# Optimization experiments

Measured on AMD Instinct MI355X. Metric: run time of the kernel, lower is better.

The kernel has to match this reference:

```python
import jax, jax.numpy as jnp
import numpy as np

N, D_IN, D_H, D_OUT, R, E, NB = 50000, 128, 128, 64, 4, 400000, 2

def _xavier(k, shape, fan_in, fan_out):
    # torch xavier_uniform with relu gain sqrt(2)
    lim = np.sqrt(2.0) * np.sqrt(6.0 / (fan_in + fan_out))
    return jax.random.uniform(k, shape, jnp.float32, -lim, lim)

def setup_inputs() -> dict:
    key = jax.random.key(0)
    ks = jax.random.split(key, 9)
    x = jax.random.normal(ks[0], (N, D_IN), dtype=jnp.float32)
    src = jax.random.randint(ks[1], (R, E), 0, N, dtype=jnp.int32)
    dst = jax.random.randint(ks[2], (R, E), 0, N, dtype=jnp.int32)
    inp = {"x": x, "src": src, "dst": dst}
    dims = [(D_IN, D_H), (D_H, D_H), (D_H, D_OUT)]
    for i, (di, do) in enumerate(dims):
        inp[f"basis{i}"] = _xavier(ks[3 + 2 * i], (NB, di, do), di, do)
        inp[f"coeff{i}"] = _xavier(ks[4 + 2 * i], (R, NB), NB, R)
    return inp

def _rel_layer(h, src, dst, basis, coeff):
    """One RelGraphConvLayer: per-relation basis weight + GraphConv(norm='both'),
    summed over relations (HeteroGraphConv aggregate='sum')."""
    n = h.shape[0]
    W = jnp.einsum('rb,bio->rio', coeff, basis)  # [R, d_in, d_out] basis-decomposed weights
    out = jnp.zeros((n, W.shape[-1]), dtype=h.dtype)
    for r in range(src.shape[0]):  # fixed small set of relations
        s, d = src[r], dst[r]
        ones = jnp.ones(s.shape[0], dtype=h.dtype)
        deg_out = jnp.maximum(jax.ops.segment_sum(ones, s, num_segments=n), 1.0)
        deg_in = jnp.maximum(jax.ops.segment_sum(ones, d, num_segments=n), 1.0)
        norm_src = deg_out ** -0.5
        norm_dst = deg_in ** -0.5
        # weight applied before aggregation (d_in >= d_out path of dgl GraphConv; math identical)
        hr = (h * norm_src[:, None]) @ W[r]            # [N, d_out]
        agg = jax.ops.segment_sum(hr[s], d, num_segments=n)  # SpMM via gather + scatter-add
        out = out + agg * norm_dst[:, None]
    return out

def reference(x, src, dst, basis0, coeff0, basis1, coeff1, basis2, coeff2):
    h = jax.nn.relu(_rel_layer(x, src, dst, basis0, coeff0))
    h = jax.nn.relu(_rel_layer(h, src, dst, basis1, coeff1))
    return _rel_layer(h, src, dst, basis2, coeff2)  # final layer: no activation
```

## Files before the change

kernel.cpp:

```cpp
#include <hip/hip_runtime.h>
#include <hip/hip_bf16.h>
#include <cstdint>
#include <cstddef>

#define NN 50000
#define RR 4
#define EE 400000
#define TE (RR*EE)
#define HR 12500
#define RN (RR*NN)
#define NSEG (NN*RR)
#define SCB2 782
#define NBK 512
#define BKSZ 98
#define CHA 4000
#define MAXSPAN 4608

using frag_ab = __attribute__((ext_vector_type(8))) short;
using frag_cd = __attribute__((ext_vector_type(4))) float;

static __device__ __forceinline__ unsigned short f2bf(float f) {
    union { float f; unsigned u; } v; v.f = f;
    unsigned r = (v.u + 0x7FFF + ((v.u >> 16) & 1)) >> 16;
    return (unsigned short)r;
}
static __device__ __forceinline__ unsigned pack2(float lo, float hi) {
    return (unsigned)f2bf(lo) | ((unsigned)f2bf(hi) << 16);
}
static __device__ __forceinline__ float blo(unsigned u) { return __uint_as_float(u << 16); }
static __device__ __forceinline__ float bhi(unsigned u) { return __uint_as_float(u & 0xFFFF0000u); }

__global__ __launch_bounds__(1024) void k_hist(const int* __restrict__ src,
                                               const int* __restrict__ dst,
                                               int* __restrict__ cnt_srcQ,
                                               int* __restrict__ cnt_dstQ) {
    __shared__ unsigned bins[HR / 2];
    int combo = blockIdx.x >> 4;
    int range = (blockIdx.x >> 2) & 3;
    int qc    = blockIdx.x & 3;
    int r = combo >> 1;
    int side = combo & 1;
    const int* arr = (side == 0 ? src : dst) + (size_t)r * EE + (size_t)qc * (EE / 4);
    int lo = range * HR;
    for (int i = threadIdx.x; i < HR / 2; i += 1024) bins[i] = 0;
    __syncthreads();
    const int4* a4 = (const int4*)arr;
    for (int i = threadIdx.x; i < EE / 16; i += 1024) {
        int4 v = a4[i];
        int t;
        t = v.x - lo; if ((unsigned)t < (unsigned)HR) atomicAdd(&bins[t >> 1], 1u << ((t & 1) * 16));
        t = v.y - lo; if ((unsigned)t < (unsigned)HR) atomicAdd(&bins[t >> 1], 1u << ((t & 1) * 16));
        t = v.z - lo; if ((unsigned)t < (unsigned)HR) atomicAdd(&bins[t >> 1], 1u << ((t & 1) * 16));
        t = v.w - lo; if ((unsigned)t < (unsigned)HR) atomicAdd(&bins[t >> 1], 1u << ((t & 1) * 16));
    }
    __syncthreads();
    int* outp = (side == 0 ? cnt_srcQ : cnt_dstQ) + (size_t)qc * RN + (size_t)r * NN + lo;
    for (int i = threadIdx.x; i < HR / 2; i += 1024) {
        unsigned b = bins[i];
        outp[2 * i]     = (int)(b & 0xFFFFu);
        outp[2 * i + 1] = (int)(b >> 16);
    }
}

__global__ __launch_bounds__(256) void k_sum_norms(const int* __restrict__ cnt_srcQ,
                                                   const int* __restrict__ cnt_dstQ,
                                                   float* __restrict__ nsrc,
                                                   float* __restrict__ ndst,
                                                   int* __restrict__ cntd2) {
    int i = blockIdx.x * 256 + threadIdx.x;
    if (i >= RN) return;
    int ss = cnt_srcQ[i] + cnt_srcQ[RN + i] + cnt_srcQ[2 * RN + i] + cnt_srcQ[3 * RN + i];
    int ds = cnt_dstQ[i] + cnt_dstQ[RN + i] + cnt_dstQ[2 * RN + i] + cnt_dstQ[3 * RN + i];
    nsrc[i] = 1.0f / sqrtf(fmaxf((float)ss, 1.0f));
    ndst[i] = 1.0f / sqrtf(fmaxf((float)ds, 1.0f));
    int r = i / NN, d = i - r * NN;
    cntd2[d * 4 + r] = ds;
}

__global__ __launch_bounds__(256) void k_partial(const int* __restrict__ cntd2,
                                                 int* __restrict__ part) {
    __shared__ int s[256];
    int t = threadIdx.x;
    int f = blockIdx.x * 256 + t;
    int v = (f < NSEG) ? cntd2[f] : 0;
    s[t] = v;
    __syncthreads();
    for (int off = 128; off > 0; off >>= 1) {
        if (t < off) s[t] += s[t + off];
        __syncthreads();
    }
    if (t == 0) part[blockIdx.x] = s[0];
}

__global__ __launch_bounds__(1024) void k_scan_small(const int* __restrict__ part,
                                                     int* __restrict__ offs) {
    __shared__ int s[1024];
    int t = threadIdx.x;
    s[t] = (t < SCB2) ? part[t] : 0;
    __syncthreads();
    for (int off = 1; off < 1024; off <<= 1) {
        int v = (t >= off) ? s[t - off] : 0;
        __syncthreads();
        s[t] += v;
        __syncthreads();
    }
    if (t < SCB2) offs[t] = (t == 0) ? 0 : s[t - 1];
}

__global__ __launch_bounds__(256) void k_emit(const int* __restrict__ cntd2,
                                              const int* __restrict__ offs,
                                              int* __restrict__ rp2) {
    __shared__ int s[256];
    int t = threadIdx.x;
    int f = blockIdx.x * 256 + t;
    int v = (f < NSEG) ? cntd2[f] : 0;
    s[t] = v;
    __syncthreads();
    for (int off = 1; off < 256; off <<= 1) {
        int u = (t >= off) ? s[t - off] : 0;
        __syncthreads();
        s[t] += u;
        __syncthreads();
    }
    if (f < NSEG) rp2[f] = offs[blockIdx.x] + s[t] - v;
    if (f == NSEG - 1) rp2[NSEG] = TE;
}

__global__ __launch_bounds__(256) void k_initg(const int* __restrict__ rp2,
                                               int* __restrict__ gcur) {
    int i = blockIdx.x * 256 + threadIdx.x;
    if (i < NBK) gcur[i] = rp2[min(i * BKSZ * 4, NSEG)];
}

__global__ __launch_bounds__(256) void k_fillA(const int* __restrict__ src,
                                               const int* __restrict__ dst,
                                               int* __restrict__ gcur,
                                               unsigned* __restrict__ stage) {
    __shared__ int cnt[NBK];
    __shared__ int rcur[NBK];
    int r = blockIdx.y;
    int base_e = blockIdx.x * CHA;
    int t = threadIdx.x;
    for (int i = t; i < NBK; i += 256) cnt[i] = 0;
    __syncthreads();
    const int* dr = dst + (size_t)r * EE;
    const int* sr = src + (size_t)r * EE;
    for (int i = base_e + t; i < base_e + CHA; i += 256) {
        int d = dr[i];
        atomicAdd(&cnt[d / BKSZ], 1);
    }
    __syncthreads();
    for (int i = t; i < NBK; i += 256) rcur[i] = atomicAdd(&gcur[i], cnt[i]);
    __syncthreads();
    for (int i = base_e + t; i < base_e + CHA; i += 256) {
        int d = dr[i];
        int s = sr[i];
        int b = d / BKSZ;
        int dl = d - b * BKSZ;
        int pos = atomicAdd(&rcur[b], 1);
        stage[pos] = (unsigned)s | ((unsigned)r << 16) | ((unsigned)dl << 18);
    }
}

__global__ __launch_bounds__(256) void k_fillB(const unsigned* __restrict__ stage,
                                               const int* __restrict__ rp2,
                                               const float* __restrict__ nsrc,
                                               const float* __restrict__ ndst,
                                               uint2* __restrict__ ed) {
    __shared__ unsigned imgU[MAXSPAN];
    __shared__ float imgW[MAXSPAN];
    __shared__ int lcur[BKSZ * 4];
    __shared__ float ndL[BKSZ * 4];
    int b = blockIdx.x;
    int t = threadIdx.x;
    int node0 = b * BKSZ;
    if (node0 >= NN) return;
    int nodes = min(BKSZ, NN - node0);
    int nseg_local = nodes * 4;
    int segbase = node0 * 4;
    for (int i = t; i < nseg_local; i += 256) {
        lcur[i] = rp2[segbase + i];
        ndL[i] = ndst[(i & 3) * NN + node0 + (i >> 2)];
    }
    __syncthreads();
    int S0 = rp2[segbase];
    int S1 = rp2[segbase + nseg_local];
    int span = S1 - S0;
    if (span <= MAXSPAN) {
        for (int i = S0 + t; i < S1; i += 256) {
            unsigned w = stage[i];
            int s = (int)(w & 0xFFFFu);
            int r = (int)((w >> 16) & 3u);
            int dl = (int)(w >> 18);
            int seg = dl * 4 + r;
            int pos = atomicAdd(&lcur[seg], 1);
            int idx = pos - S0;
            imgU[idx] = w & 0x3FFFFu;
            imgW[idx] = nsrc[r * NN + s] * ndL[seg];
        }
        __syncthreads();
        for (int i = t; i < span; i += 256)
            ed[S0 + i] = make_uint2(imgU[i], __float_as_uint(imgW[i]));
    } else {
        for (int i = S0 + t; i < S1; i += 256) {
            unsigned w = stage[i];
            int s = (int)(w & 0xFFFFu);
            int r = (int)((w >> 16) & 3u);
            int dl = (int)(w >> 18);
            int seg = dl * 4 + r;
            int pos = atomicAdd(&lcur[seg], 1);
            ed[pos] = make_uint2(w & 0x3FFFFu,
                                 __float_as_uint(nsrc[r * NN + s] * ndL[seg]));
        }
    }
}

__global__ __launch_bounds__(256) void k_cvt_x(const float4* __restrict__ x4,
                                               uint2* __restrict__ o, int n4) {
    int i = blockIdx.x * 256 + threadIdx.x;
    if (i >= n4) return;
    float4 v = x4[i];
    o[i] = make_uint2(pack2(v.x, v.y), pack2(v.z, v.w));
}

__global__ __launch_bounds__(256) void k_cvt_bt(const float* __restrict__ B,
                                                unsigned short* __restrict__ Bt, int BN) {
    int o = blockIdx.x * 256 + threadIdx.x;
    if (o >= BN * 256) return;
    int k = o & 255, n = o >> 8;
    Bt[o] = f2bf(B[k * BN + n]);
}

__global__ __launch_bounds__(256) void k_agg(const uint4* __restrict__ hb4,
                                             const int* __restrict__ rp2,
                                             const uint2* __restrict__ ed,
                                             const float* __restrict__ coeff,
                                             uint2* __restrict__ Mb2) {
    int wave = (blockIdx.x * 256 + threadIdx.x) >> 6;
    int lane = threadIdx.x & 63;
    if (wave >= NN) return;
    int q = lane >> 4, hl = lane & 15;

    float c00 = coeff[0], c01 = coeff[1], c10 = coeff[2], c11 = coeff[3];
    float c20 = coeff[4], c21 = coeff[5], c30 = coeff[6], c31 = coeff[7];

    float a00 = 0.f, a01 = 0.f, a02 = 0.f, a03 = 0.f;
    float a04 = 0.f, a05 = 0.f, a06 = 0.f, a07 = 0.f;
    float a10 = 0.f, a11 = 0.f, a12 = 0.f, a13 = 0.f;
    float a14 = 0.f, a15 = 0.f, a16 = 0.f, a17 = 0.f;

    int e0 = rp2[wave * 4], e1 = rp2[wave * 4 + 4];

    int e = e0;
    for (; e + 7 < e1; e += 8) {
        uint2 weA = ed[e + q];
        uint2 weB = ed[e + 4 + q];
        uint4 hA = hb4[(size_t)(weA.x & 0xFFFFu) * 16 + hl];
        uint4 hB = hb4[(size_t)(weB.x & 0xFFFFu) * 16 + hl];
        int rA = (int)(weA.x >> 16);
        int rB = (int)(weB.x >> 16);
        float wsA = __uint_as_float(weA.y);
        float wsB = __uint_as_float(weB.y);
        float wa0 = (rA == 0 ? c00 : rA == 1 ? c10 : rA == 2 ? c20 : c30) * wsA;
        float wa1 = (rA == 0 ? c01 : rA == 1 ? c11 : rA == 2 ? c21 : c31) * wsA;
        float wb0 = (rB == 0 ? c00 : rB == 1 ? c10 : rB == 2 ? c20 : c30) * wsB;
        float wb1 = (rB == 0 ? c01 : rB == 1 ? c11 : rB == 2 ? c21 : c31) * wsB;

        float h0 = blo(hA.x), h1 = bhi(hA.x), h2 = blo(hA.y), h3 = bhi(hA.y);
        float h4 = blo(hA.z), h5 = bhi(hA.z), h6 = blo(hA.w), h7 = bhi(hA.w);
        a00 += wa0 * h0; a01 += wa0 * h1; a02 += wa0 * h2; a03 += wa0 * h3;
        a04 += wa0 * h4; a05 += wa0 * h5; a06 += wa0 * h6; a07 += wa0 * h7;
        a10 += wa1 * h0; a11 += wa1 * h1; a12 += wa1 * h2; a13 += wa1 * h3;
        a14 += wa1 * h4; a15 += wa1 * h5; a16 += wa1 * h6; a17 += wa1 * h7;

        h0 = blo(hB.x); h1 = bhi(hB.x); h2 = blo(hB.y); h3 = bhi(hB.y);
        h4 = blo(hB.z); h5 = bhi(hB.z); h6 = blo(hB.w); h7 = bhi(hB.w);
        a00 += wb0 * h0; a01 += wb0 * h1; a02 += wb0 * h2; a03 += wb0 * h3;
        a04 += wb0 * h4; a05 += wb0 * h5; a06 += wb0 * h6; a07 += wb0 * h7;
        a10 += wb1 * h0; a11 += wb1 * h1; a12 += wb1 * h2; a13 += wb1 * h3;
        a14 += wb1 * h4; a15 += wb1 * h5; a16 += wb1 * h6; a17 += wb1 * h7;
    }
    for (; e < e1; e += 4) {
        int E = e + q;
        bool act = E < e1;
        uint2 weA = ed[act ? E : e0];
        uint4 hA = hb4[(size_t)(weA.x & 0xFFFFu) * 16 + hl];
        int rA = (int)(weA.x >> 16);
        float wsA = act ? __uint_as_float(weA.y) : 0.f;
        float wa0 = (rA == 0 ? c00 : rA == 1 ? c10 : rA == 2 ? c20 : c30) * wsA;
        float wa1 = (rA == 0 ? c01 : rA == 1 ? c11 : rA == 2 ? c21 : c31) * wsA;
        float h0 = blo(hA.x), h1 = bhi(hA.x), h2 = blo(hA.y), h3 = bhi(hA.y);
        float h4 = blo(hA.z), h5 = bhi(hA.z), h6 = blo(hA.w), h7 = bhi(hA.w);
        a00 += wa0 * h0; a01 += wa0 * h1; a02 += wa0 * h2; a03 += wa0 * h3;
        a04 += wa0 * h4; a05 += wa0 * h5; a06 += wa0 * h6; a07 += wa0 * h7;
        a10 += wa1 * h0; a11 += wa1 * h1; a12 += wa1 * h2; a13 += wa1 * h3;
        a14 += wa1 * h4; a15 += wa1 * h5; a16 += wa1 * h6; a17 += wa1 * h7;
    }

    a00 += __shfl_xor(a00, 16, 64); a00 += __shfl_xor(a00, 32, 64);
    a01 += __shfl_xor(a01, 16, 64); a01 += __shfl_xor(a01, 32, 64);
    a02 += __shfl_xor(a02, 16, 64); a02 += __shfl_xor(a02, 32, 64);
    a03 += __shfl_xor(a03, 16, 64); a03 += __shfl_xor(a03, 32, 64);
    a04 += __shfl_xor(a04, 16, 64); a04 += __shfl_xor(a04, 32, 64);
    a05 += __shfl_xor(a05, 16, 64); a05 += __shfl_xor(a05, 32, 64);
    a06 += __shfl_xor(a06, 16, 64); a06 += __shfl_xor(a06, 32, 64);
    a07 += __shfl_xor(a07, 16, 64); a07 += __shfl_xor(a07, 32, 64);
    a10 += __shfl_xor(a10, 16, 64); a10 += __shfl_xor(a10, 32, 64);
    a11 += __shfl_xor(a11, 16, 64); a11 += __shfl_xor(a11, 32, 64);
    a12 += __shfl_xor(a12, 16, 64); a12 += __shfl_xor(a12, 32, 64);
    a13 += __shfl_xor(a13, 16, 64); a13 += __shfl_xor(a13, 32, 64);
    a14 += __shfl_xor(a14, 16, 64); a14 += __shfl_xor(a14, 32, 64);
    a15 += __shfl_xor(a15, 16, 64); a15 += __shfl_xor(a15, 32, 64);
    a16 += __shfl_xor(a16, 16, 64); a16 += __shfl_xor(a16, 32, 64);
    a17 += __shfl_xor(a17, 16, 64); a17 += __shfl_xor(a17, 32, 64);

    int c = q >> 1, h4 = q & 1;
    float v0 = c ? (h4 ? a14 : a10) : (h4 ? a04 : a00);
    float v1 = c ? (h4 ? a15 : a11) : (h4 ? a05 : a01);
    float v2 = c ? (h4 ? a16 : a12) : (h4 ? a06 : a02);
    float v3 = c ? (h4 ? a17 : a13) : (h4 ? a07 : a03);
    uint2 st;
    st.x = pack2(v0, v1);
    st.y = pack2(v2, v3);
    Mb2[(size_t)wave * 64 + c * 32 + hl * 2 + h4] = st;
}

template <int BN, bool BF16OUT>
__global__ __launch_bounds__(256) void k_gemm(const unsigned short* __restrict__ A,
                                              const unsigned short* __restrict__ Bt,
                                              void* __restrict__ Cout) {
    int wave = threadIdx.x >> 6, lane = threadIdx.x & 63;
    int row0 = blockIdx.x * 64 + wave * 16;
    if (row0 >= NN) return;
    int m = lane & 15, q = lane >> 4;
    const int NT = BN / 16;

    frag_cd acc[NT];
#pragma unroll
    for (int ct = 0; ct < NT; ct++) acc[ct] = (frag_cd){0.f, 0.f, 0.f, 0.f};

    const size_t abase = (size_t)(row0 + m) * 256 + q * 8;
#pragma unroll
    for (int kc = 0; kc < 8; kc++) {
        frag_ab a = *(const frag_ab*)(A + abase + kc * 32);
#pragma unroll
        for (int ct = 0; ct < NT; ct++) {
            frag_ab b = *(const frag_ab*)(Bt + (size_t)(ct * 16 + m) * 256 + kc * 32 + q * 8);
            acc[ct] = __builtin_amdgcn_mfma_f32_16x16x32_bf16(a, b, acc[ct], 0, 0, 0);
        }
    }

#pragma unroll
    for (int ct = 0; ct < NT; ct++) {
#pragma unroll
        for (int i = 0; i < 4; i++) {
            int row = row0 + q * 4 + i;
            int col = ct * 16 + m;
            float v = acc[ct][i];
            if (BF16OUT) {
                v = fmaxf(v, 0.f);
                ((unsigned short*)Cout)[(size_t)row * BN + col] = f2bf(v);
            } else {
                ((float*)Cout)[(size_t)row * BN + col] = v;
            }
        }
    }
}


extern "C" void kernel_launch(void* const* d_in, const int* in_sizes, int n_in,
                              void* d_out, int out_size, void* d_ws, size_t ws_size,
                              hipStream_t stream) {
    const float* x      = (const float*)d_in[0];
    const int*   src    = (const int*)d_in[1];
    const int*   dst    = (const int*)d_in[2];
    const float* basis0 = (const float*)d_in[3];
    const float* coeff0 = (const float*)d_in[4];
    const float* basis1 = (const float*)d_in[5];
    const float* coeff1 = (const float*)d_in[6];
    const float* basis2 = (const float*)d_in[7];
    const float* coeff2 = (const float*)d_in[8];
    float* out = (float*)d_out;

    char* p = (char*)d_ws;
    auto alloc = [&](size_t bytes) {
        char* r = p;
        p += (bytes + 255) & ~(size_t)255;
        return r;
    };
    int*   cnt_srcQ = (int*)alloc((size_t)4 * RN * 4);
    int*   cnt_dstQ = (int*)alloc((size_t)4 * RN * 4);
    float* nsrc     = (float*)alloc((size_t)RN * 4);
    float* ndst     = (float*)alloc((size_t)RN * 4);
    int*   cntd2    = (int*)alloc((size_t)NSEG * 4);
    int*   rp2      = (int*)alloc((size_t)(NSEG + 1) * 4);
    int*   part     = (int*)alloc((size_t)SCB2 * 4);
    int*   offs     = (int*)alloc((size_t)SCB2 * 4);
    int*   gcur     = (int*)alloc((size_t)NBK * 4);
    unsigned* stage = (unsigned*)alloc((size_t)TE * 4);
    uint2* ed       = (uint2*)alloc((size_t)TE * 8);
    unsigned* Mb   = (unsigned*)alloc((size_t)NN * 128 * 4);
    unsigned* Hb   = (unsigned*)alloc((size_t)NN * 64 * 4);
    unsigned* Xb   = (unsigned*)alloc((size_t)NN * 64 * 4);
    unsigned short* Bt0 = (unsigned short*)alloc((size_t)128 * 256 * 2);
    unsigned short* Bt1 = (unsigned short*)alloc((size_t)128 * 256 * 2);
    unsigned short* Bt2 = (unsigned short*)alloc((size_t)64 * 256 * 2);

    k_cvt_x<<<(NN * 32 + 255) / 256, 256, 0, stream>>>((const float4*)x, (uint2*)Xb, NN * 32);
    k_cvt_bt<<<(128 * 256 + 255) / 256, 256, 0, stream>>>(basis0, Bt0, 128);
    k_cvt_bt<<<(128 * 256 + 255) / 256, 256, 0, stream>>>(basis1, Bt1, 128);
    k_cvt_bt<<<(64 * 256 + 255) / 256, 256, 0, stream>>>(basis2, Bt2, 64);
    k_hist<<<128, 1024, 0, stream>>>(src, dst, cnt_srcQ, cnt_dstQ);
    k_sum_norms<<<(RN + 255) / 256, 256, 0, stream>>>(cnt_srcQ, cnt_dstQ, nsrc, ndst, cntd2);
    k_partial<<<SCB2, 256, 0, stream>>>(cntd2, part);
    k_scan_small<<<1, 1024, 0, stream>>>(part, offs);
    k_emit<<<SCB2, 256, 0, stream>>>(cntd2, offs, rp2);
    k_initg<<<(NBK + 255) / 256, 256, 0, stream>>>(rp2, gcur);
    k_fillA<<<dim3(EE / CHA, RR), 256, 0, stream>>>(src, dst, gcur, stage);
    k_fillB<<<NBK, 256, 0, stream>>>(stage, rp2, nsrc, ndst, ed);

    int aggBlocks = NN / 4;
    int gemmBlocks = (NN + 63) / 64;

    k_agg<<<aggBlocks, 256, 0, stream>>>((const uint4*)Xb, rp2, ed, coeff0, (uint2*)Mb);
    k_gemm<128, true><<<gemmBlocks, 256, 0, stream>>>((const unsigned short*)Mb, Bt0, Hb);
    k_agg<<<aggBlocks, 256, 0, stream>>>((const uint4*)Hb, rp2, ed, coeff1, (uint2*)Mb);
    k_gemm<128, true><<<gemmBlocks, 256, 0, stream>>>((const unsigned short*)Mb, Bt1, Hb);
    k_agg<<<aggBlocks, 256, 0, stream>>>((const uint4*)Hb, rp2, ed, coeff2, (uint2*)Mb);
    k_gemm<64, false><<<gemmBlocks, 256, 0, stream>>>((const unsigned short*)Mb, Bt2, out);
}
```

Before: 415.1 us.

## Precompute per-layer coeff-scaled bf16 edge weights and fuse setup kernels

```diff
diff --git a/kernel.cpp b/kernel.cpp
--- a/kernel.cpp
+++ b/kernel.cpp
@@ -7,7 +7,7 @@
 #define RR 4
 #define EE 400000
 #define TE (RR*EE)
-#define HR 12500
+#define HR2 25000
 #define RN (RR*NN)
 #define NSEG (NN*RR)
 #define SCB2 782
@@ -15,6 +15,7 @@
 #define BKSZ 98
 #define CHA 4000
 #define MAXSPAN 4608
+#define XBLK 6250
 
 using frag_ab = __attribute__((ext_vector_type(8))) short;
 using frag_cd = __attribute__((ext_vector_type(4))) float;
@@ -34,28 +35,28 @@
                                                const int* __restrict__ dst,
                                                int* __restrict__ cnt_srcQ,
                                                int* __restrict__ cnt_dstQ) {
-    __shared__ unsigned bins[HR / 2];
-    int combo = blockIdx.x >> 4;
-    int range = (blockIdx.x >> 2) & 3;
+    __shared__ unsigned bins[HR2 / 2];
+    int combo = blockIdx.x >> 3;
+    int range = (blockIdx.x >> 2) & 1;
     int qc    = blockIdx.x & 3;
     int r = combo >> 1;
     int side = combo & 1;
     const int* arr = (side == 0 ? src : dst) + (size_t)r * EE + (size_t)qc * (EE / 4);
-    int lo = range * HR;
-    for (int i = threadIdx.x; i < HR / 2; i += 1024) bins[i] = 0;
+    int lo = range * HR2;
+    for (int i = threadIdx.x; i < HR2 / 2; i += 1024) bins[i] = 0;
     __syncthreads();
     const int4* a4 = (const int4*)arr;
     for (int i = threadIdx.x; i < EE / 16; i += 1024) {
         int4 v = a4[i];
         int t;
-        t = v.x - lo; if ((unsigned)t < (unsigned)HR) atomicAdd(&bins[t >> 1], 1u << ((t & 1) * 16));
-        t = v.y - lo; if ((unsigned)t < (unsigned)HR) atomicAdd(&bins[t >> 1], 1u << ((t & 1) * 16));
-        t = v.z - lo; if ((unsigned)t < (unsigned)HR) atomicAdd(&bins[t >> 1], 1u << ((t & 1) * 16));
-        t = v.w - lo; if ((unsigned)t < (unsigned)HR) atomicAdd(&bins[t >> 1], 1u << ((t & 1) * 16));
+        t = v.x - lo; if ((unsigned)t < (unsigned)HR2) atomicAdd(&bins[t >> 1], 1u << ((t & 1) * 16));
+        t = v.y - lo; if ((unsigned)t < (unsigned)HR2) atomicAdd(&bins[t >> 1], 1u << ((t & 1) * 16));
+        t = v.z - lo; if ((unsigned)t < (unsigned)HR2) atomicAdd(&bins[t >> 1], 1u << ((t & 1) * 16));
+        t = v.w - lo; if ((unsigned)t < (unsigned)HR2) atomicAdd(&bins[t >> 1], 1u << ((t & 1) * 16));
     }
     __syncthreads();
     int* outp = (side == 0 ? cnt_srcQ : cnt_dstQ) + (size_t)qc * RN + (size_t)r * NN + lo;
-    for (int i = threadIdx.x; i < HR / 2; i += 1024) {
+    for (int i = threadIdx.x; i < HR2 / 2; i += 1024) {
         unsigned b = bins[i];
         outp[2 * i]     = (int)(b & 0xFFFFu);
         outp[2 * i + 1] = (int)(b >> 16);
@@ -109,7 +110,8 @@
 
 __global__ __launch_bounds__(256) void k_emit(const int* __restrict__ cntd2,
                                               const int* __restrict__ offs,
-                                              int* __restrict__ rp2) {
+                                              int* __restrict__ rp2,
+                                              int* __restrict__ gcur) {
     __shared__ int s[256];
     int t = threadIdx.x;
     int f = blockIdx.x * 256 + t;
@@ -122,14 +124,12 @@
         s[t] += u;
         __syncthreads();
     }
-    if (f < NSEG) rp2[f] = offs[blockIdx.x] + s[t] - v;
+    if (f < NSEG) {
+        int ex = offs[blockIdx.x] + s[t] - v;
+        rp2[f] = ex;
+        if (f % (BKSZ * 4) == 0) gcur[f / (BKSZ * 4)] = ex;
+    }
     if (f == NSEG - 1) rp2[NSEG] = TE;
-}
-
-__global__ __launch_bounds__(256) void k_initg(const int* __restrict__ rp2,
-                                               int* __restrict__ gcur) {
-    int i = blockIdx.x * 256 + threadIdx.x;
-    if (i < NBK) gcur[i] = rp2[min(i * BKSZ * 4, NSEG)];
 }
 
 __global__ __launch_bounds__(256) void k_fillA(const int* __restrict__ src,
@@ -150,7 +150,7 @@
         atomicAdd(&cnt[d / BKSZ], 1);
     }
     __syncthreads();
-    for (int i = t; i < NBK; i += 256) rcur[i] = atomicAdd(&gcur[i], cnt[i]);
+    for (int i = t; i < NBK; i += 256) rcur[i] = (i * BKSZ < NN) ? atomicAdd(&gcur[i], cnt[i]) : 0;
     __syncthreads();
     for (int i = base_e + t; i < base_e + CHA; i += 256) {
         int d = dr[i];
@@ -166,7 +166,10 @@
                                                const int* __restrict__ rp2,
                                                const float* __restrict__ nsrc,
                                                const float* __restrict__ ndst,
-                                               uint2* __restrict__ ed) {
+                                               const float* __restrict__ c0p,
+                                               const float* __restrict__ c1p,
+                                               const float* __restrict__ c2p,
+                                               uint4* __restrict__ ed) {
     __shared__ unsigned imgU[MAXSPAN];
     __shared__ float imgW[MAXSPAN];
     __shared__ int lcur[BKSZ * 4];
@@ -175,6 +178,12 @@
     int t = threadIdx.x;
     int node0 = b * BKSZ;
     if (node0 >= NN) return;
+    float c00 = c0p[0], c01 = c0p[1], c02 = c0p[2], c03 = c0p[3];
+    float c04 = c0p[4], c05 = c0p[5], c06 = c0p[6], c07 = c0p[7];
+    float c10 = c1p[0], c11 = c1p[1], c12 = c1p[2], c13 = c1p[3];
+    float c14 = c1p[4], c15 = c1p[5], c16 = c1p[6], c17 = c1p[7];
+    float c20 = c2p[0], c21 = c2p[1], c22 = c2p[2], c23 = c2p[3];
+    float c24 = c2p[4], c25 = c2p[5], c26 = c2p[6], c27 = c2p[7];
     int nodes = min(BKSZ, NN - node0);
     int nseg_local = nodes * 4;
     int segbase = node0 * 4;
@@ -199,8 +208,18 @@
             imgW[idx] = nsrc[r * NN + s] * ndL[seg];
         }
         __syncthreads();
-        for (int i = t; i < span; i += 256)
-            ed[S0 + i] = make_uint2(imgU[i], __float_as_uint(imgW[i]));
+        for (int i = t; i < span; i += 256) {
+            unsigned u = imgU[i];
+            float w = imgW[i];
+            int r = (int)(u >> 16);
+            float wa = (r == 0 ? c00 : r == 1 ? c02 : r == 2 ? c04 : c06) * w;
+            float wb = (r == 0 ? c01 : r == 1 ? c03 : r == 2 ? c05 : c07) * w;
+            float wc = (r == 0 ? c10 : r == 1 ? c12 : r == 2 ? c14 : c16) * w;
+            float wd = (r == 0 ? c11 : r == 1 ? c13 : r == 2 ? c15 : c17) * w;
+            float we = (r == 0 ? c20 : r == 1 ? c22 : r == 2 ? c24 : c26) * w;
+            float wf = (r == 0 ? c21 : r == 1 ? c23 : r == 2 ? c25 : c27) * w;
+            ed[S0 + i] = make_uint4(u & 0xFFFFu, pack2(wa, wb), pack2(wc, wd), pack2(we, wf));
+        }
     } else {
         for (int i = S0 + t; i < S1; i += 256) {
             unsigned w = stage[i];
@@ -209,41 +228,57 @@
             int dl = (int)(w >> 18);
             int seg = dl * 4 + r;
             int pos = atomicAdd(&lcur[seg], 1);
-            ed[pos] = make_uint2(w & 0x3FFFFu,
-                                 __float_as_uint(nsrc[r * NN + s] * ndL[seg]));
+            float ww = nsrc[r * NN + s] * ndL[seg];
+            float wa = (r == 0 ? c00 : r == 1 ? c02 : r == 2 ? c04 : c06) * ww;
+            float wb = (r == 0 ? c01 : r == 1 ? c03 : r == 2 ? c05 : c07) * ww;
+            float wc = (r == 0 ? c10 : r == 1 ? c12 : r == 2 ? c14 : c16) * ww;
+            float wd = (r == 0 ? c11 : r == 1 ? c13 : r == 2 ? c15 : c17) * ww;
+            float we = (r == 0 ? c20 : r == 1 ? c22 : r == 2 ? c24 : c26) * ww;
+            float wf = (r == 0 ? c21 : r == 1 ? c23 : r == 2 ? c25 : c27) * ww;
+            ed[pos] = make_uint4((unsigned)s, pack2(wa, wb), pack2(wc, wd), pack2(we, wf));
         }
     }
 }
 
-__global__ __launch_bounds__(256) void k_cvt_x(const float4* __restrict__ x4,
-                                               uint2* __restrict__ o, int n4) {
-    int i = blockIdx.x * 256 + threadIdx.x;
-    if (i >= n4) return;
-    float4 v = x4[i];
-    o[i] = make_uint2(pack2(v.x, v.y), pack2(v.z, v.w));
-}
-
-__global__ __launch_bounds__(256) void k_cvt_bt(const float* __restrict__ B,
-                                                unsigned short* __restrict__ Bt, int BN) {
-    int o = blockIdx.x * 256 + threadIdx.x;
-    if (o >= BN * 256) return;
-    int k = o & 255, n = o >> 8;
-    Bt[o] = f2bf(B[k * BN + n]);
-}
-
+__global__ __launch_bounds__(256) void k_cvt_all(const float4* __restrict__ x4,
+                                                 const float* __restrict__ B0,
+                                                 const float* __restrict__ B1,
+                                                 const float* __restrict__ B2,
+                                                 uint2* __restrict__ Xb,
+                                                 unsigned short* __restrict__ Bt0,
+                                                 unsigned short* __restrict__ Bt1,
+                                                 unsigned short* __restrict__ Bt2) {
+    int b = blockIdx.x;
+    int t = threadIdx.x;
+    if (b < XBLK) {
+        int i = b * 256 + t;
+        float4 v = x4[i];
+        Xb[i] = make_uint2(pack2(v.x, v.y), pack2(v.z, v.w));
+    } else if (b < XBLK + 128) {
+        int o = (b - XBLK) * 256 + t;
+        int k = o & 255, n = o >> 8;
+        Bt0[o] = f2bf(B0[k * 128 + n]);
+    } else if (b < XBLK + 256) {
+        int o = (b - XBLK - 128) * 256 + t;
+        int k = o & 255, n = o >> 8;
+        Bt1[o] = f2bf(B1[k * 128 + n]);
+    } else {
+        int o = (b - XBLK - 256) * 256 + t;
+        int k = o & 255, n = o >> 8;
+        Bt2[o] = f2bf(B2[k * 64 + n]);
+    }
+}
+
+template <int L>
 __global__ __launch_bounds__(256) void k_agg(const uint4* __restrict__ hb4,
                                              const int* __restrict__ rp2,
-                                             const uint2* __restrict__ ed,
-                                             const float* __restrict__ coeff,
+                                             const uint4* __restrict__ ed,
                                              uint2* __restrict__ Mb2) {
     int wave = (blockIdx.x * 256 + threadIdx.x) >> 6;
     int lane = threadIdx.x & 63;
     if (wave >= NN) return;
     int q = lane >> 4, hl = lane & 15;
 
-    float c00 = coeff[0], c01 = coeff[1], c10 = coeff[2], c11 = coeff[3];
-    float c20 = coeff[4], c21 = coeff[5], c30 = coeff[6], c31 = coeff[7];
-
     float a00 = 0.f, a01 = 0.f, a02 = 0.f, a03 = 0.f;
     float a04 = 0.f, a05 = 0.f, a06 = 0.f, a07 = 0.f;
     float a10 = 0.f, a11 = 0.f, a12 = 0.f, a13 = 0.f;
@@ -252,49 +287,66 @@
     int e0 = rp2[wave * 4], e1 = rp2[wave * 4 + 4];
 
     int e = e0;
-    for (; e + 7 < e1; e += 8) {
-        uint2 weA = ed[e + q];
-        uint2 weB = ed[e + 4 + q];
-        uint4 hA = hb4[(size_t)(weA.x & 0xFFFFu) * 16 + hl];
-        uint4 hB = hb4[(size_t)(weB.x & 0xFFFFu) * 16 + hl];
-        int rA = (int)(weA.x >> 16);
-        int rB = (int)(weB.x >> 16);
-        float wsA = __uint_as_float(weA.y);
-        float wsB = __uint_as_float(weB.y);
-        float wa0 = (rA == 0 ? c00 : rA == 1 ? c10 : rA == 2 ? c20 : c30) * wsA;
-        float wa1 = (rA == 0 ? c01 : rA == 1 ? c11 : rA == 2 ? c21 : c31) * wsA;
-        float wb0 = (rB == 0 ? c00 : rB == 1 ? c10 : rB == 2 ? c20 : c30) * wsB;
-        float wb1 = (rB == 0 ? c01 : rB == 1 ? c11 : rB == 2 ? c21 : c31) * wsB;
+    for (; e + 15 < e1; e += 16) {
+        uint4 pA = ed[e + q];
+        uint4 pB = ed[e + 4 + q];
+        uint4 pC = ed[e + 8 + q];
+        uint4 pD = ed[e + 12 + q];
+        uint4 hA = hb4[(size_t)pA.x * 16 + hl];
+        uint4 hB = hb4[(size_t)pB.x * 16 + hl];
+        uint4 hC = hb4[(size_t)pC.x * 16 + hl];
+        uint4 hD = hb4[(size_t)pD.x * 16 + hl];
+        unsigned kA = (L == 0) ? pA.y : (L == 1) ? pA.z : pA.w;
+        unsigned kB = (L == 0) ? pB.y : (L == 1) ? pB.z : pB.w;
+        unsigned kC = (L == 0) ? pC.y : (L == 1) ? pC.z : pC.w;
+        unsigned kD = (L == 0) ? pD.y : (L == 1) ? pD.z : pD.w;
+        float wA0 = blo(kA), wA1 = bhi(kA);
+        float wB0 = blo(kB), wB1 = bhi(kB);
+        float wC0 = blo(kC), wC1 = bhi(kC);
+        float wD0 = blo(kD), wD1 = bhi(kD);
 
         float h0 = blo(hA.x), h1 = bhi(hA.x), h2 = blo(hA.y), h3 = bhi(hA.y);
         float h4 = blo(hA.z), h5 = bhi(hA.z), h6 = blo(hA.w), h7 = bhi(hA.w);
-        a00 += wa0 * h0; a01 += wa0 * h1; a02 += wa0 * h2; a03 += wa0 * h3;
-        a04 += wa0 * h4; a05 += wa0 * h5; a06 += wa0 * h6; a07 += wa0 * h7;
-        a10 += wa1 * h0; a11 += wa1 * h1; a12 += wa1 * h2; a13 += wa1 * h3;
-        a14 += wa1 * h4; a15 += wa1 * h5; a16 += wa1 * h6; a17 += wa1 * h7;
+        a00 += wA0 * h0; a01 += wA0 * h1; a02 += wA0 * h2; a03 += wA0 * h3;
+        a04 += wA0 * h4; a05 += wA0 * h5; a06 += wA0 * h6; a07 += wA0 * h7;
+        a10 += wA1 * h0; a11 += wA1 * h1; a12 += wA1 * h2; a13 += wA1 * h3;
+        a14 += wA1 * h4; a15 += wA1 * h5; a16 += wA1 * h6; a17 += wA1 * h7;
 
         h0 = blo(hB.x); h1 = bhi(hB.x); h2 = blo(hB.y); h3 = bhi(hB.y);
         h4 = blo(hB.z); h5 = bhi(hB.z); h6 = blo(hB.w); h7 = bhi(hB.w);
-        a00 += wb0 * h0; a01 += wb0 * h1; a02 += wb0 * h2; a03 += wb0 * h3;
-        a04 += wb0 * h4; a05 += wb0 * h5; a06 += wb0 * h6; a07 += wb0 * h7;
-        a10 += wb1 * h0; a11 += wb1 * h1; a12 += wb1 * h2; a13 += wb1 * h3;
-        a14 += wb1 * h4; a15 += wb1 * h5; a16 += wb1 * h6; a17 += wb1 * h7;
+        a00 += wB0 * h0; a01 += wB0 * h1; a02 += wB0 * h2; a03 += wB0 * h3;
+        a04 += wB0 * h4; a05 += wB0 * h5; a06 += wB0 * h6; a07 += wB0 * h7;
+        a10 += wB1 * h0; a11 += wB1 * h1; a12 += wB1 * h2; a13 += wB1 * h3;
+        a14 += wB1 * h4; a15 += wB1 * h5; a16 += wB1 * h6; a17 += wB1 * h7;
+
+        h0 = blo(hC.x); h1 = bhi(hC.x); h2 = blo(hC.y); h3 = bhi(hC.y);
+        h4 = blo(hC.z); h5 = bhi(hC.z); h6 = blo(hC.w); h7 = bhi(hC.w);
+        a00 += wC0 * h0; a01 += wC0 * h1; a02 += wC0 * h2; a03 += wC0 * h3;
+        a04 += wC0 * h4; a05 += wC0 * h5; a06 += wC0 * h6; a07 += wC0 * h7;
+        a10 += wC1 * h0; a11 += wC1 * h1; a12 += wC1 * h2; a13 += wC1 * h3;
+        a14 += wC1 * h4; a15 += wC1 * h5; a16 += wC1 * h6; a17 += wC1 * h7;
+
+        h0 = blo(hD.x); h1 = bhi(hD.x); h2 = blo(hD.y); h3 = bhi(hD.y);
+        h4 = blo(hD.z); h5 = bhi(hD.z); h6 = blo(hD.w); h7 = bhi(hD.w);
+        a00 += wD0 * h0; a01 += wD0 * h1; a02 += wD0 * h2; a03 += wD0 * h3;
+        a04 += wD0 * h4; a05 += wD0 * h5; a06 += wD0 * h6; a07 += wD0 * h7;
+        a10 += wD1 * h0; a11 += wD1 * h1; a12 += wD1 * h2; a13 += wD1 * h3;
+        a14 += wD1 * h4; a15 += wD1 * h5; a16 += wD1 * h6; a17 += wD1 * h7;
     }
     for (; e < e1; e += 4) {
         int E = e + q;
         bool act = E < e1;
-        uint2 weA = ed[act ? E : e0];
-        uint4 hA = hb4[(size_t)(weA.x & 0xFFFFu) * 16 + hl];
-        int rA = (int)(weA.x >> 16);
-        float wsA = act ? __uint_as_float(weA.y) : 0.f;
-        float wa0 = (rA == 0 ? c00 : rA == 1 ? c10 : rA == 2 ? c20 : c30) * wsA;
-        float wa1 = (rA == 0 ? c01 : rA == 1 ? c11 : rA == 2 ? c21 : c31) * wsA;
+        uint4 pA = ed[act ? E : e0];
+        uint4 hA = hb4[(size_t)pA.x * 16 + hl];
+        unsigned kA = (L == 0) ? pA.y : (L == 1) ? pA.z : pA.w;
+        float wA0 = act ? blo(kA) : 0.f;
+        float wA1 = act ? bhi(kA) : 0.f;
         float h0 = blo(hA.x), h1 = bhi(hA.x), h2 = blo(hA.y), h3 = bhi(hA.y);
         float h4 = blo(hA.z), h5 = bhi(hA.z), h6 = blo(hA.w), h7 = bhi(hA.w);
-        a00 += wa0 * h0; a01 += wa0 * h1; a02 += wa0 * h2; a03 += wa0 * h3;
-        a04 += wa0 * h4; a05 += wa0 * h5; a06 += wa0 * h6; a07 += wa0 * h7;
-        a10 += wa1 * h0; a11 += wa1 * h1; a12 += wa1 * h2; a13 += wa1 * h3;
-        a14 += wa1 * h4; a15 += wa1 * h5; a16 += wa1 * h6; a17 += wa1 * h7;
+        a00 += wA0 * h0; a01 += wA0 * h1; a02 += wA0 * h2; a03 += wA0 * h3;
+        a04 += wA0 * h4; a05 += wA0 * h5; a06 += wA0 * h6; a07 += wA0 * h7;
+        a10 += wA1 * h0; a11 += wA1 * h1; a12 += wA1 * h2; a13 += wA1 * h3;
+        a14 += wA1 * h4; a15 += wA1 * h5; a16 += wA1 * h6; a17 += wA1 * h7;
     }
 
     a00 += __shfl_xor(a00, 16, 64); a00 += __shfl_xor(a00, 32, 64);
@@ -398,7 +450,7 @@
     int*   offs     = (int*)alloc((size_t)SCB2 * 4);
     int*   gcur     = (int*)alloc((size_t)NBK * 4);
     unsigned* stage = (unsigned*)alloc((size_t)TE * 4);
-    uint2* ed       = (uint2*)alloc((size_t)TE * 8);
+    uint4* ed       = (uint4*)alloc((size_t)TE * 16);
     unsigned* Mb   = (unsigned*)alloc((size_t)NN * 128 * 4);
     unsigned* Hb   = (unsigned*)alloc((size_t)NN * 64 * 4);
     unsigned* Xb   = (unsigned*)alloc((size_t)NN * 64 * 4);
@@ -406,26 +458,23 @@
     unsigned short* Bt1 = (unsigned short*)alloc((size_t)128 * 256 * 2);
     unsigned short* Bt2 = (unsigned short*)alloc((size_t)64 * 256 * 2);
 
-    k_cvt_x<<<(NN * 32 + 255) / 256, 256, 0, stream>>>((const float4*)x, (uint2*)Xb, NN * 32);
-    k_cvt_bt<<<(128 * 256 + 255) / 256, 256, 0, stream>>>(basis0, Bt0, 128);
-    k_cvt_bt<<<(128 * 256 + 255) / 256, 256, 0, stream>>>(basis1, Bt1, 128);
-    k_cvt_bt<<<(64 * 256 + 255) / 256, 256, 0, stream>>>(basis2, Bt2, 64);
-    k_hist<<<128, 1024, 0, stream>>>(src, dst, cnt_srcQ, cnt_dstQ);
+    k_cvt_all<<<XBLK + 320, 256, 0, stream>>>((const float4*)x, basis0, basis1, basis2,
+                                              (uint2*)Xb, Bt0, Bt1, Bt2);
+    k_hist<<<64, 1024, 0, stream>>>(src, dst, cnt_srcQ, cnt_dstQ);
     k_sum_norms<<<(RN + 255) / 256, 256, 0, stream>>>(cnt_srcQ, cnt_dstQ, nsrc, ndst, cntd2);
     k_partial<<<SCB2, 256, 0, stream>>>(cntd2, part);
     k_scan_small<<<1, 1024, 0, stream>>>(part, offs);
-    k_emit<<<SCB2, 256, 0, stream>>>(cntd2, offs, rp2);
-    k_initg<<<(NBK + 255) / 256, 256, 0, stream>>>(rp2, gcur);
+    k_emit<<<SCB2, 256, 0, stream>>>(cntd2, offs, rp2, gcur);
     k_fillA<<<dim3(EE / CHA, RR), 256, 0, stream>>>(src, dst, gcur, stage);
-    k_fillB<<<NBK, 256, 0, stream>>>(stage, rp2, nsrc, ndst, ed);
+    k_fillB<<<NBK, 256, 0, stream>>>(stage, rp2, nsrc, ndst, coeff0, coeff1, coeff2, ed);
 
     int aggBlocks = NN / 4;
     int gemmBlocks = (NN + 63) / 64;
 
-    k_agg<<<aggBlocks, 256, 0, stream>>>((const uint4*)Xb, rp2, ed, coeff0, (uint2*)Mb);
+    k_agg<0><<<aggBlocks, 256, 0, stream>>>((const uint4*)Xb, rp2, ed, (uint2*)Mb);
     k_gemm<128, true><<<gemmBlocks, 256, 0, stream>>>((const unsigned short*)Mb, Bt0, Hb);
-    k_agg<<<aggBlocks, 256, 0, stream>>>((const uint4*)Hb, rp2, ed, coeff1, (uint2*)Mb);
+    k_agg<1><<<aggBlocks, 256, 0, stream>>>((const uint4*)Hb, rp2, ed, (uint2*)Mb);
     k_gemm<128, true><<<gemmBlocks, 256, 0, stream>>>((const unsigned short*)Mb, Bt1, Hb);
-    k_agg<<<aggBlocks, 256, 0, stream>>>((const uint4*)Hb, rp2, ed, coeff2, (uint2*)Mb);
+    k_agg<2><<<aggBlocks, 256, 0, stream>>>((const uint4*)Hb, rp2, ed, (uint2*)Mb);
     k_gemm<64, false><<<gemmBlocks, 256, 0, stream>>>((const unsigned short*)Mb, Bt2, out);
 }
```

New measurement: 415.4 us. About the same (+0.1%).
